# Optimization experiments

Hardware: AMD Instinct MI355X
Metric: run time of the kernel (lower is better)

## Reference

```python
import jax, jax.numpy as jnp
import numpy as np

D_MODEL = 1024
H = 16
D_K = D_MODEL // H


def setup_inputs() -> dict:
    key = jax.random.key(0)
    ks = jax.random.split(key, 12)
    B, S = 2, 2048
    scale = 1.0 / np.sqrt(D_MODEL)
    inp = {
        "q": jax.random.normal(ks[0], (B, S, D_MODEL), jnp.float32),
        "k": jax.random.normal(ks[1], (B, S, D_MODEL), jnp.float32),
        "v": jax.random.normal(ks[2], (B, S, D_MODEL), jnp.float32),
        "mask": jnp.ones((B, 1, S, S), jnp.int32),
        "w_q": jax.random.normal(ks[3], (D_MODEL, D_MODEL), jnp.float32) * scale,
        "b_q": jnp.zeros((D_MODEL,), jnp.float32),
        "w_k": jax.random.normal(ks[4], (D_MODEL, D_MODEL), jnp.float32) * scale,
        "b_k": jnp.zeros((D_MODEL,), jnp.float32),
        "w_v": jax.random.normal(ks[5], (D_MODEL, D_MODEL), jnp.float32) * scale,
        "b_v": jnp.zeros((D_MODEL,), jnp.float32),
        "w_o": jax.random.normal(ks[6], (D_MODEL, D_MODEL), jnp.float32) * scale,
        "b_o": jnp.zeros((D_MODEL,), jnp.float32),
    }
    return inp


def _split_heads(x):
    B, S, _ = x.shape
    return x.reshape(B, S, H, D_K).transpose(0, 2, 1, 3)  # [B,H,S,Dk]


def reference(q, k, v, mask, w_q, b_q, w_k, b_k, w_v, b_v, w_o, b_o):
    # Linear projections (torch Linear: x @ W^T + b)
    query = _split_heads(q @ w_q.T + b_q)
    key = _split_heads(k @ w_k.T + b_k)
    value = _split_heads(v @ w_v.T + b_v)

    # scaled dot-product attention: [B,H,S,S]
    scores = jnp.einsum("bhqd,bhkd->bhqk", query, key) / jnp.sqrt(
        jnp.asarray(D_K, query.dtype)
    )
    scores = jnp.where(mask == 0, jnp.asarray(-1e9, scores.dtype), scores)
    attn = jax.nn.softmax(scores, axis=-1)  # dropout p=0.0 -> identity
    out = jnp.einsum("bhqk,bhkd->bhqd", attn, value)  # [B,H,S,Dk]

    # combine heads -> [B,S,D_MODEL]
    B = out.shape[0]
    out = out.transpose(0, 2, 1, 3).reshape(B, -1, D_MODEL)
    return out @ w_o.T + b_o
```

## Files before the change

### kernel.cpp

```cpp
#include <hip/hip_runtime.h>
#include <hip/hip_bf16.h>

#define S_LEN 2048
#define BATCH 2
#define NH    16
#define DK    64
#define DM    1024

typedef __bf16 bf16x8 __attribute__((ext_vector_type(8)));
typedef float  f32x4  __attribute__((ext_vector_type(4)));
typedef ushort u16x8  __attribute__((ext_vector_type(8)));

__device__ __forceinline__ float bf2f(ushort u) {
    union { unsigned int i; float f; } v; v.i = ((unsigned int)u) << 16; return v.f;
}
__device__ __forceinline__ ushort f2bf(float f) {
    union { float f; unsigned int i; } v; v.f = f;
    unsigned int u = v.i;
    unsigned int r = u + 0x7fff + ((u >> 16) & 1);
    return (ushort)(r >> 16);
}

__device__ __forceinline__ void async_copy16(const ushort* g, ushort* l) {
    __builtin_amdgcn_global_load_lds(
        (__attribute__((address_space(1))) void*)(g),
        (__attribute__((address_space(3))) void*)(l), 16, 0, 0);
}

__global__ void detect(const ushort* __restrict__ q, int* __restrict__ flags) {
    __shared__ int red[256];
    int tid = threadIdx.x;
    int cnt = 0;
    for (int i = tid; i < 2048; i += 256) {
        ushort e = q[2 * i];
        int ex = (e >> 7) & 0xFF;
        if (ex == 0 || (ex >= 107 && ex <= 147)) cnt++;
    }
    red[tid] = cnt;
    __syncthreads();
    for (int s = 128; s > 0; s >>= 1) {
        if (tid < s) red[tid] += red[tid + s];
        __syncthreads();
    }
    if (tid == 0) {
        flags[0] = (red[0] < 1229) ? 1 : 0;
        flags[1] = 0;
    }
}

__global__ void mask_check(const int* __restrict__ mask, int* __restrict__ flags) {
    const int total = BATCH * S_LEN * S_LEN / 4;
    int idx = blockIdx.x * blockDim.x + threadIdx.x;
    int stride = gridDim.x * blockDim.x;
    bool bad = false;
    for (int i = idx; i < total; i += stride) {
        int4 v = ((const int4*)mask)[i];
        if (v.x == 0 || v.y == 0 || v.z == 0 || v.w == 0) bad = true;
    }
    if (__any(bad)) {
        if ((threadIdx.x & 63) == 0) atomicOr(&flags[1], 1);
    }
}

#define NJOBS 11
struct CvtJobs { const void* src[NJOBS]; };

__device__ __constant__ const int g_cum[NJOBS + 1] = {
    0, 4194304, 8388608, 12582912, 13631488, 14680064, 15728640,
    16777216, 16778240, 16779264, 16780288, 16781312
};

__global__ __launch_bounds__(256) void convert_all(CvtJobs J, ushort* __restrict__ conv,
                                                   const int* __restrict__ flags) {
    bool isf32 = flags[0] != 0;
    const int total_chunks = 16781312 / 8;
    int c = blockIdx.x * blockDim.x + threadIdx.x;
    int stride = gridDim.x * blockDim.x;
    for (; c < total_chunks; c += stride) {
        int e = c * 8;
        int j = 0;
        while (j + 1 < NJOBS + 1 && e >= g_cum[j + 1]) j++;
        int local = e - g_cum[j];
        if (isf32) {
            const float* s = (const float*)J.src[j] + local;
            f32x4 a = *(const f32x4*)s;
            f32x4 b = *(const f32x4*)(s + 4);
            ushort o[8] = { f2bf(a[0]), f2bf(a[1]), f2bf(a[2]), f2bf(a[3]),
                            f2bf(b[0]), f2bf(b[1]), f2bf(b[2]), f2bf(b[3]) };
            *(ushort4*)&conv[e]     = *(ushort4*)&o[0];
            *(ushort4*)&conv[e + 4] = *(ushort4*)&o[4];
        } else {
            const ushort* s = (const ushort*)J.src[j] + local;
            bf16x8 v = *(const bf16x8*)s;
            *(bf16x8*)&conv[e] = v;
        }
    }
}

struct GArg { const ushort* x; const ushort* w; const ushort* bias; void* y; int split; float scale; };

__global__ __launch_bounds__(256) void gemm_bt(GArg a0, GArg a1, GArg a2,
                                               const int* __restrict__ flags) {
    GArg A = (blockIdx.z == 0) ? a0 : (blockIdx.z == 1 ? a1 : a2);
    const int K = 1024, N = 1024;
    __shared__ ushort As[2][128 * 32];
    __shared__ ushort Bs[2][128 * 32];

    int tid = threadIdx.x;
    int w = tid >> 6, lane = tid & 63;
    int wm = (w >> 1) * 64, wn = (w & 1) * 64;

    int id = blockIdx.x + 8 * blockIdx.y;
    int m0 = (id & 31) * 128;
    int n0 = (id >> 5) * 128;

    f32x4 acc[4][4] = {};

    int srow0 = w * 16 + (lane >> 2);
    int srow1 = (w + 4) * 16 + (lane >> 2);
    int schunk = ((lane & 3) ^ ((lane >> 3) & 3)) * 8;

    int fr = lane & 15;
    int qd = lane >> 4;
    int fcp = (qd ^ ((fr >> 1) & 3)) * 8;

    const ushort* xr0 = A.x + (size_t)(m0 + srow0) * K + schunk;
    const ushort* xr1 = A.x + (size_t)(m0 + srow1) * K + schunk;
    const ushort* wr0 = A.w + (size_t)(n0 + srow0) * K + schunk;
    const ushort* wr1 = A.w + (size_t)(n0 + srow1) * K + schunk;

    async_copy16(xr0, &As[0][w * 512]);
    async_copy16(xr1, &As[0][(w + 4) * 512]);
    async_copy16(wr0, &Bs[0][w * 512]);
    async_copy16(wr1, &Bs[0][(w + 4) * 512]);

    for (int k = 0; k < 32; k++) {
        __syncthreads();
        int cur = k & 1, nxt = cur ^ 1;

        bf16x8 af[4], bfr[4];
#pragma unroll
        for (int i = 0; i < 4; i++) {
            af[i]  = *(const bf16x8*)&As[cur][(wm + i * 16 + fr) * 32 + fcp];
            bfr[i] = *(const bf16x8*)&Bs[cur][(wn + i * 16 + fr) * 32 + fcp];
        }

        if (k + 1 < 32) {
            int off = (k + 1) * 32;
            async_copy16(xr0 + off, &As[nxt][w * 512]);
            async_copy16(xr1 + off, &As[nxt][(w + 4) * 512]);
            async_copy16(wr0 + off, &Bs[nxt][w * 512]);
            async_copy16(wr1 + off, &Bs[nxt][(w + 4) * 512]);
        }

#pragma unroll
        for (int i = 0; i < 4; i++)
#pragma unroll
            for (int j = 0; j < 4; j++)
                acc[i][j] = __builtin_amdgcn_mfma_f32_16x16x32_bf16(af[i], bfr[j], acc[i][j], 0, 0, 0);
    }

    bool isf32 = flags[0] != 0;
    int crow = qd * 4;
    int ccol = fr;
#pragma unroll
    for (int j = 0; j < 4; j++) {
        int n_g = n0 + wn + j * 16 + ccol;
        float bias = bf2f(A.bias[n_g]);
#pragma unroll
        for (int i = 0; i < 4; i++) {
#pragma unroll
            for (int r = 0; r < 4; r++) {
                int m_g = m0 + wm + i * 16 + crow + r;
                float val = (acc[i][j][r] + bias) * A.scale;
                if (A.split) {
                    int bb = m_g >> 11, s = m_g & 2047;
                    int h = n_g >> 6, d = n_g & 63;
                    ((ushort*)A.y)[((size_t)(bb * NH + h) * S_LEN + s) * DK + d] = f2bf(val);
                } else if (isf32) {
                    ((float*)A.y)[(size_t)m_g * N + n_g] = val;
                } else {
                    ((ushort*)A.y)[(size_t)m_g * N + n_g] = f2bf(val);
                }
            }
        }
    }
}

#define VSTR 72
#define PSTR 76

__global__ __launch_bounds__(256) void attn(const ushort* __restrict__ qp,
                                            const ushort* __restrict__ kp,
                                            const ushort* __restrict__ vp,
                                            const int* __restrict__ mask,
                                            const int* __restrict__ flags,
                                            ushort* __restrict__ ctx) {
    __shared__ ushort Ks[64 * 64];
    __shared__ ushort Vt[64 * VSTR];
    __shared__ ushort Pb[4][32 * PSTR];

    int tid = threadIdx.x, w = tid >> 6, lane = tid & 63;
    int id = blockIdx.x + 16 * blockIdx.y;
    int bh = id & 31;
    int b = bh >> 4, h = bh & 15;
    int q0 = (id >> 5) * 128;

    const ushort* qb = qp + (size_t)bh * S_LEN * DK;
    const ushort* kb = kp + (size_t)bh * S_LEN * DK;
    const ushort* vb = vp + (size_t)bh * S_LEN * DK;
    const int* mb = mask + (size_t)b * S_LEN * S_LEN;
    bool do_mask = flags[1] != 0;

    int fr = lane & 15;
    int qd = lane >> 4;

    bf16x8 qf[2][2];
#pragma unroll
    for (int rt = 0; rt < 2; rt++)
#pragma unroll
        for (int kc = 0; kc < 2; kc++)
            qf[rt][kc] = *(const bf16x8*)&qb[(size_t)(q0 + w * 32 + rt * 16 + fr) * DK + kc * 32 + qd * 8];

    bf16x8 ones;
#pragma unroll
    for (int j = 0; j < 8; j++) ones[j] = (__bf16)1.0f;

    f32x4 oacc[2][4] = {};
    f32x4 lacc[2] = {};

    int kschunk = ((lane & 7) ^ ((lane >> 3) & 7)) * 8;
    int ksrow0 = w * 8 + (lane >> 3);
    int ksrow1 = (w + 4) * 8 + (lane >> 3);
    int vc0 = w * 8, vc1 = (w + 4) * 8;

    for (int k0 = 0; k0 < S_LEN; k0 += 64) {
        u16x8 vx0 = *(const u16x8*)&vb[(size_t)(k0 + lane) * DK + vc0];
        u16x8 vx1 = *(const u16x8*)&vb[(size_t)(k0 + lane) * DK + vc1];
        __syncthreads();
        async_copy16(&kb[(size_t)(k0 + ksrow0) * DK + kschunk], &Ks[w * 512]);
        async_copy16(&kb[(size_t)(k0 + ksrow1) * DK + kschunk], &Ks[(w + 4) * 512]);
#pragma unroll
        for (int j = 0; j < 8; j++) {
            Vt[(vc0 + j) * VSTR + lane] = vx0[j];
            Vt[(vc1 + j) * VSTR + lane] = vx1[j];
        }
        __syncthreads();

        f32x4 sc[2][4] = {};
#pragma unroll
        for (int kc = 0; kc < 2; kc++) {
            bf16x8 kf[4];
#pragma unroll
            for (int ct = 0; ct < 4; ct++) {
                int key = ct * 16 + fr;
                kf[ct] = *(const bf16x8*)&Ks[key * 64 + (((kc * 4 + qd) ^ (fr & 7)) * 8)];
            }
#pragma unroll
            for (int rt = 0; rt < 2; rt++)
#pragma unroll
                for (int ct = 0; ct < 4; ct++)
                    sc[rt][ct] = __builtin_amdgcn_mfma_f32_16x16x32_bf16(qf[rt][kc], kf[ct], sc[rt][ct], 0, 0, 0);
        }

        if (do_mask) {
#pragma unroll
            for (int rt = 0; rt < 2; rt++)
#pragma unroll
                for (int ct = 0; ct < 4; ct++)
#pragma unroll
                    for (int r = 0; r < 4; r++) {
                        int qr = q0 + w * 32 + rt * 16 + qd * 4 + r;
                        int kcid = k0 + ct * 16 + fr;
                        if (mb[(size_t)qr * S_LEN + kcid] == 0) sc[rt][ct][r] = -1e9f;
                    }
        }

#pragma unroll
        for (int rt = 0; rt < 2; rt++)
#pragma unroll
            for (int ct = 0; ct < 4; ct++)
#pragma unroll
                for (int r = 0; r < 4; r++) {
                    union { float f; ushort2 hh; } t;
                    t.f = __builtin_amdgcn_exp2f(sc[rt][ct][r]);
                    Pb[w][(rt * 16 + qd * 4 + r) * PSTR + ct * 16 + fr] = t.hh.y;
                }

#pragma unroll
        for (int kk = 0; kk < 2; kk++) {
            bf16x8 pf[2], vf[4];
#pragma unroll
            for (int rt = 0; rt < 2; rt++)
                pf[rt] = *(const bf16x8*)&Pb[w][(rt * 16 + fr) * PSTR + kk * 32 + qd * 8];
#pragma unroll
            for (int dt = 0; dt < 4; dt++)
                vf[dt] = *(const bf16x8*)&Vt[(dt * 16 + fr) * VSTR + kk * 32 + qd * 8];
#pragma unroll
            for (int rt = 0; rt < 2; rt++) {
                lacc[rt] = __builtin_amdgcn_mfma_f32_16x16x32_bf16(pf[rt], ones, lacc[rt], 0, 0, 0);
#pragma unroll
                for (int dt = 0; dt < 4; dt++)
                    oacc[rt][dt] = __builtin_amdgcn_mfma_f32_16x16x32_bf16(pf[rt], vf[dt], oacc[rt][dt], 0, 0, 0);
            }
        }
    }

#pragma unroll
    for (int rt = 0; rt < 2; rt++)
#pragma unroll
        for (int r = 0; r < 4; r++) {
            float inv = 1.0f / lacc[rt][r];
            int qr = q0 + w * 32 + rt * 16 + qd * 4 + r;
            size_t rowbase = ((size_t)(b * S_LEN + qr) * NH + h) * DK;
#pragma unroll
            for (int dt = 0; dt < 4; dt++)
                ctx[rowbase + dt * 16 + fr] = f2bf(oacc[rt][dt][r] * inv);
        }
}

extern "C" void kernel_launch(void* const* d_in, const int* in_sizes, int n_in,
                              void* d_out, int out_size, void* d_ws, size_t ws_size,
                              hipStream_t stream) {
    const int* mask = (const int*)d_in[3];

    char* ws = (char*)d_ws;
    int*    flags = (int*)ws;
    ushort* conv  = (ushort*)(ws + 4096);
    const size_t conv_bytes = 16781312ull * 2;
    char* p = ws + 4096 + ((conv_bytes + 4095) & ~4095ull);
    size_t sz = (size_t)BATCH * NH * S_LEN * DK * sizeof(ushort);
    ushort* qp  = (ushort*)(p);
    ushort* kp  = (ushort*)(p + sz);
    ushort* vp  = (ushort*)(p + 2 * sz);
    ushort* ctx = (ushort*)(p + 3 * sz);

    ushort* qc  = conv + 0;
    ushort* kc  = conv + 4194304;
    ushort* vc  = conv + 8388608;
    ushort* wqc = conv + 12582912;
    ushort* wkc = conv + 13631488;
    ushort* wvc = conv + 14680064;
    ushort* woc = conv + 15728640;
    ushort* bqc = conv + 16777216;
    ushort* bkc = conv + 16778240;
    ushort* bvc = conv + 16779264;
    ushort* boc = conv + 16780288;

    detect<<<1, 256, 0, stream>>>((const ushort*)d_in[0], flags);
    mask_check<<<1024, 256, 0, stream>>>(mask, flags);

    CvtJobs J;
    J.src[0] = d_in[0];  J.src[1] = d_in[1];  J.src[2] = d_in[2];
    J.src[3] = d_in[4];  J.src[4] = d_in[6];  J.src[5] = d_in[8];
    J.src[6] = d_in[10]; J.src[7] = d_in[5];  J.src[8] = d_in[7];
    J.src[9] = d_in[9];  J.src[10] = d_in[11];
    convert_all<<<2048, 256, 0, stream>>>(J, conv, flags);

    const float cs = 0.125f * 1.44269504f;
    GArg aq{qc, wqc, bqc, qp, 1, cs};
    GArg ak{kc, wkc, bkc, kp, 1, 1.0f};
    GArg av{vc, wvc, bvc, vp, 1, 1.0f};
    gemm_bt<<<dim3(8, 32, 3), 256, 0, stream>>>(aq, ak, av, flags);

    attn<<<dim3(16, 32), 256, 0, stream>>>(qp, kp, vp, mask, flags, ctx);

    GArg ao{ctx, woc, boc, d_out, 0, 1.0f};
    gemm_bt<<<dim3(8, 32, 1), 256, 0, stream>>>(ao, ao, ao, flags);
}
```

Before: 278.6 us.

## Write V transposed from projection GEMM and stream K/V fragments directly from global

The V projection epilogue now writes V in a head-transposed [B,H,Dk,S] layout with vectorized 4-element stores. The attention kernel drops the shared-memory K and V tiles and both block barriers, loading K fragments straight from global with one-tile register prefetch and reading transposed V fragments directly. The QK^T MFMA operands are swapped so each lane owns a query row, which enables packed P stores and row-contiguous mask reads. s_setprio wraps the MFMA sections. The risks are more global-load latency exposed per wave, since K/V are no longer shared across the block, and higher register pressure.

Result: slower. 333.7 us (+19.8%).

```diff
diff --git a/kernel.cpp b/kernel.cpp
--- a/kernel.cpp
+++ b/kernel.cpp
@@ -19,6 +19,10 @@
     unsigned int u = v.i;
     unsigned int r = u + 0x7fff + ((u >> 16) & 1);
     return (ushort)(r >> 16);
+}
+__device__ __forceinline__ unsigned int packbf(float a, float b) {
+    union { float f; unsigned int u; } x, y; x.f = a; y.f = b;
+    return (x.u >> 16) | (y.u & 0xFFFF0000u);
 }
 
 __device__ __forceinline__ void async_copy16(const ushort* g, ushort* l) {
@@ -169,25 +173,36 @@
         float bias = bf2f(A.bias[n_g]);
 #pragma unroll
         for (int i = 0; i < 4; i++) {
-#pragma unroll
-            for (int r = 0; r < 4; r++) {
-                int m_g = m0 + wm + i * 16 + crow + r;
-                float val = (acc[i][j][r] + bias) * A.scale;
-                if (A.split) {
-                    int bb = m_g >> 11, s = m_g & 2047;
-                    int h = n_g >> 6, d = n_g & 63;
-                    ((ushort*)A.y)[((size_t)(bb * NH + h) * S_LEN + s) * DK + d] = f2bf(val);
-                } else if (isf32) {
-                    ((float*)A.y)[(size_t)m_g * N + n_g] = val;
-                } else {
-                    ((ushort*)A.y)[(size_t)m_g * N + n_g] = f2bf(val);
+            if (A.split == 2) {
+                ushort4 o;
+                o.x = f2bf((acc[i][j][0] + bias) * A.scale);
+                o.y = f2bf((acc[i][j][1] + bias) * A.scale);
+                o.z = f2bf((acc[i][j][2] + bias) * A.scale);
+                o.w = f2bf((acc[i][j][3] + bias) * A.scale);
+                int m_g0 = m0 + wm + i * 16 + crow;
+                int bb = m_g0 >> 11, s = m_g0 & 2047;
+                int h = n_g >> 6, d = n_g & 63;
+                *(ushort4*)&((ushort*)A.y)[((size_t)(bb * NH + h) * DK + d) * S_LEN + s] = o;
+            } else {
+#pragma unroll
+                for (int r = 0; r < 4; r++) {
+                    int m_g = m0 + wm + i * 16 + crow + r;
+                    float val = (acc[i][j][r] + bias) * A.scale;
+                    if (A.split) {
+                        int bb = m_g >> 11, s = m_g & 2047;
+                        int h = n_g >> 6, d = n_g & 63;
+                        ((ushort*)A.y)[((size_t)(bb * NH + h) * S_LEN + s) * DK + d] = f2bf(val);
+                    } else if (isf32) {
+                        ((float*)A.y)[(size_t)m_g * N + n_g] = val;
+                    } else {
+                        ((ushort*)A.y)[(size_t)m_g * N + n_g] = f2bf(val);
+                    }
                 }
             }
         }
     }
 }
 
-#define VSTR 72
 #define PSTR 76
 
 __global__ __launch_bounds__(256) void attn(const ushort* __restrict__ qp,
@@ -196,8 +211,6 @@
                                             const int* __restrict__ mask,
                                             const int* __restrict__ flags,
                                             ushort* __restrict__ ctx) {
-    __shared__ ushort Ks[64 * 64];
-    __shared__ ushort Vt[64 * VSTR];
     __shared__ ushort Pb[4][32 * PSTR];
 
     int tid = threadIdx.x, w = tid >> 6, lane = tid & 63;
@@ -206,9 +219,9 @@
     int b = bh >> 4, h = bh & 15;
     int q0 = (id >> 5) * 128;
 
-    const ushort* qb = qp + (size_t)bh * S_LEN * DK;
-    const ushort* kb = kp + (size_t)bh * S_LEN * DK;
-    const ushort* vb = vp + (size_t)bh * S_LEN * DK;
+    const ushort* qb  = qp + (size_t)bh * S_LEN * DK;
+    const ushort* kb  = kp + (size_t)bh * S_LEN * DK;
+    const ushort* vtb = vp + (size_t)bh * DK * S_LEN;
     const int* mb = mask + (size_t)b * S_LEN * S_LEN;
     bool do_mask = flags[1] != 0;
 
@@ -229,81 +242,86 @@
     f32x4 oacc[2][4] = {};
     f32x4 lacc[2] = {};
 
-    int kschunk = ((lane & 7) ^ ((lane >> 3) & 7)) * 8;
-    int ksrow0 = w * 8 + (lane >> 3);
-    int ksrow1 = (w + 4) * 8 + (lane >> 3);
-    int vc0 = w * 8, vc1 = (w + 4) * 8;
+    bf16x8 kf[2][4];
+#pragma unroll
+    for (int kc = 0; kc < 2; kc++)
+#pragma unroll
+        for (int ct = 0; ct < 4; ct++)
+            kf[kc][ct] = *(const bf16x8*)&kb[(size_t)(ct * 16 + fr) * DK + kc * 32 + qd * 8];
 
     for (int k0 = 0; k0 < S_LEN; k0 += 64) {
-        u16x8 vx0 = *(const u16x8*)&vb[(size_t)(k0 + lane) * DK + vc0];
-        u16x8 vx1 = *(const u16x8*)&vb[(size_t)(k0 + lane) * DK + vc1];
-        __syncthreads();
-        async_copy16(&kb[(size_t)(k0 + ksrow0) * DK + kschunk], &Ks[w * 512]);
-        async_copy16(&kb[(size_t)(k0 + ksrow1) * DK + kschunk], &Ks[(w + 4) * 512]);
-#pragma unroll
-        for (int j = 0; j < 8; j++) {
-            Vt[(vc0 + j) * VSTR + lane] = vx0[j];
-            Vt[(vc1 + j) * VSTR + lane] = vx1[j];
-        }
-        __syncthreads();
-
         f32x4 sc[2][4] = {};
-#pragma unroll
-        for (int kc = 0; kc < 2; kc++) {
-            bf16x8 kf[4];
+        __builtin_amdgcn_s_setprio(1);
+#pragma unroll
+        for (int kc = 0; kc < 2; kc++)
+#pragma unroll
+            for (int rt = 0; rt < 2; rt++)
+#pragma unroll
+                for (int ct = 0; ct < 4; ct++)
+                    sc[rt][ct] = __builtin_amdgcn_mfma_f32_16x16x32_bf16(kf[kc][ct], qf[rt][kc], sc[rt][ct], 0, 0, 0);
+        __builtin_amdgcn_s_setprio(0);
+
+        bf16x8 vf[2][4];
+#pragma unroll
+        for (int kk = 0; kk < 2; kk++)
+#pragma unroll
+            for (int dt = 0; dt < 4; dt++)
+                vf[kk][dt] = *(const bf16x8*)&vtb[(size_t)(dt * 16 + fr) * S_LEN + k0 + kk * 32 + qd * 8];
+
+        if (k0 + 64 < S_LEN) {
+            int kn = k0 + 64;
+#pragma unroll
+            for (int kc = 0; kc < 2; kc++)
+#pragma unroll
+                for (int ct = 0; ct < 4; ct++)
+                    kf[kc][ct] = *(const bf16x8*)&kb[(size_t)(kn + ct * 16 + fr) * DK + kc * 32 + qd * 8];
+        }
+
+        if (do_mask) {
+#pragma unroll
+            for (int rt = 0; rt < 2; rt++) {
+                int qr = q0 + w * 32 + rt * 16 + fr;
+                const int* mrow = &mb[(size_t)qr * S_LEN + k0];
+#pragma unroll
+                for (int ct = 0; ct < 4; ct++)
+#pragma unroll
+                    for (int r = 0; r < 4; r++)
+                        if (mrow[ct * 16 + qd * 4 + r] == 0) sc[rt][ct][r] = -1e9f;
+            }
+        }
+
+#pragma unroll
+        for (int rt = 0; rt < 2; rt++)
 #pragma unroll
             for (int ct = 0; ct < 4; ct++) {
-                int key = ct * 16 + fr;
-                kf[ct] = *(const bf16x8*)&Ks[key * 64 + (((kc * 4 + qd) ^ (fr & 7)) * 8)];
+                float p0 = __builtin_amdgcn_exp2f(sc[rt][ct][0]);
+                float p1 = __builtin_amdgcn_exp2f(sc[rt][ct][1]);
+                float p2 = __builtin_amdgcn_exp2f(sc[rt][ct][2]);
+                float p3 = __builtin_amdgcn_exp2f(sc[rt][ct][3]);
+                uint2 pk;
+                pk.x = packbf(p0, p1);
+                pk.y = packbf(p2, p3);
+                *(uint2*)&Pb[w][(rt * 16 + fr) * PSTR + ct * 16 + qd * 4] = pk;
             }
+
+        bf16x8 pf[2][2];
+#pragma unroll
+        for (int kk = 0; kk < 2; kk++)
 #pragma unroll
             for (int rt = 0; rt < 2; rt++)
-#pragma unroll
-                for (int ct = 0; ct < 4; ct++)
-                    sc[rt][ct] = __builtin_amdgcn_mfma_f32_16x16x32_bf16(qf[rt][kc], kf[ct], sc[rt][ct], 0, 0, 0);
-        }
-
-        if (do_mask) {
-#pragma unroll
-            for (int rt = 0; rt < 2; rt++)
-#pragma unroll
-                for (int ct = 0; ct < 4; ct++)
-#pragma unroll
-                    for (int r = 0; r < 4; r++) {
-                        int qr = q0 + w * 32 + rt * 16 + qd * 4 + r;
-                        int kcid = k0 + ct * 16 + fr;
-                        if (mb[(size_t)qr * S_LEN + kcid] == 0) sc[rt][ct][r] = -1e9f;
-                    }
-        }
-
-#pragma unroll
-        for (int rt = 0; rt < 2; rt++)
-#pragma unroll
-            for (int ct = 0; ct < 4; ct++)
-#pragma unroll
-                for (int r = 0; r < 4; r++) {
-                    union { float f; ushort2 hh; } t;
-                    t.f = __builtin_amdgcn_exp2f(sc[rt][ct][r]);
-                    Pb[w][(rt * 16 + qd * 4 + r) * PSTR + ct * 16 + fr] = t.hh.y;
-                }
-
-#pragma unroll
-        for (int kk = 0; kk < 2; kk++) {
-            bf16x8 pf[2], vf[4];
-#pragma unroll
-            for (int rt = 0; rt < 2; rt++)
-                pf[rt] = *(const bf16x8*)&Pb[w][(rt * 16 + fr) * PSTR + kk * 32 + qd * 8];
-#pragma unroll
-            for (int dt = 0; dt < 4; dt++)
-                vf[dt] = *(const bf16x8*)&Vt[(dt * 16 + fr) * VSTR + kk * 32 + qd * 8];
+                pf[kk][rt] = *(const bf16x8*)&Pb[w][(rt * 16 + fr) * PSTR + kk * 32 + qd * 8];
+
+        __builtin_amdgcn_s_setprio(1);
+#pragma unroll
+        for (int kk = 0; kk < 2; kk++)
 #pragma unroll
             for (int rt = 0; rt < 2; rt++) {
-                lacc[rt] = __builtin_amdgcn_mfma_f32_16x16x32_bf16(pf[rt], ones, lacc[rt], 0, 0, 0);
+                lacc[rt] = __builtin_amdgcn_mfma_f32_16x16x32_bf16(pf[kk][rt], ones, lacc[rt], 0, 0, 0);
 #pragma unroll
                 for (int dt = 0; dt < 4; dt++)
-                    oacc[rt][dt] = __builtin_amdgcn_mfma_f32_16x16x32_bf16(pf[rt], vf[dt], oacc[rt][dt], 0, 0, 0);
+                    oacc[rt][dt] = __builtin_amdgcn_mfma_f32_16x16x32_bf16(pf[kk][rt], vf[kk][dt], oacc[rt][dt], 0, 0, 0);
             }
-        }
+        __builtin_amdgcn_s_setprio(0);
     }
 
 #pragma unroll
@@ -360,7 +378,7 @@
     const float cs = 0.125f * 1.44269504f;
     GArg aq{qc, wqc, bqc, qp, 1, cs};
     GArg ak{kc, wkc, bkc, kp, 1, 1.0f};
-    GArg av{vc, wvc, bvc, vp, 1, 1.0f};
+    GArg av{vc, wvc, bvc, vp, 2, 1.0f};
     gemm_bt<<<dim3(8, 32, 3), 256, 0, stream>>>(aq, ak, av, flags);
 
     attn<<<dim3(16, 32), 256, 0, stream>>>(qp, kp, vp, mask, flags, ctx);
```
